# Optimization experiments

Hardware: AMD Instinct MI355X
Metric: run time of the kernel (lower is better)

## Reference

```python
import jax, jax.numpy as jnp
import numpy as np
import math

D_MODEL = 1024
N_HEADS = 16
HEAD_DIM = D_MODEL // N_HEADS


def setup_inputs() -> dict:
    key = jax.random.key(0)
    k1, k2, k3 = jax.random.split(key, 3)
    B, T = 2, 2048
    x = jax.random.normal(k1, (B, T, D_MODEL), dtype=jnp.float32)
    W_qkv = jax.random.normal(k2, (D_MODEL, 3 * D_MODEL), dtype=jnp.float32) * (1.0 / math.sqrt(D_MODEL))
    W_out = jax.random.normal(k3, (D_MODEL, D_MODEL), dtype=jnp.float32) * (1.0 / math.sqrt(D_MODEL))
    return {"x": x, "W_qkv": W_qkv, "W_out": W_out}


def reference(x, W_qkv, W_out):
    B, T, C = x.shape
    qkv = x @ W_qkv  # [B, T, 3C]
    q, k, v = jnp.split(qkv, 3, axis=-1)

    def heads(t):  # [B,T,C] -> [B,H,T,Dh]
        return t.reshape(B, T, N_HEADS, HEAD_DIM).transpose(0, 2, 1, 3)

    q, k, v = heads(q), heads(k), heads(v)
    scale = 1.0 / math.sqrt(HEAD_DIM)
    scores = jnp.einsum('bhtd,bhsd->bhts', q, k) * scale  # [B,H,T,T]
    causal = jnp.tril(jnp.ones((T, T), dtype=bool))
    scores = jnp.where(causal[None, None, :, :], scores, -jnp.inf)
    attn = jax.nn.softmax(scores, axis=-1)
    out = jnp.einsum('bhts,bhsd->bhtd', attn, v)  # [B,H,T,Dh]
    out = out.transpose(0, 2, 1, 3).reshape(B, T, C)
    return out @ W_out
```

## Files before the change

### kernel.cpp

```cpp
#include <hip/hip_runtime.h>
#include <hip/hip_bf16.h>

typedef __bf16 bf16;
typedef bf16 bf16x4 __attribute__((ext_vector_type(4)));
typedef bf16 bf16x8 __attribute__((ext_vector_type(8)));
typedef float f32x4 __attribute__((ext_vector_type(4)));

#define GLOAD16(g, l) __builtin_amdgcn_global_load_lds( \
    (const __attribute__((address_space(1))) void*)(g),  \
    (__attribute__((address_space(3))) void*)(l), 16, 0, 0)

#define EXP2F(x) __builtin_amdgcn_exp2f(x)
#define MFMA16(a, b, c) __builtin_amdgcn_mfma_f32_16x16x32_bf16(a, b, c, 0, 0, 0)

__global__ __launch_bounds__(256) void prep(const float* __restrict__ x,
                                            const float* __restrict__ Wqkv,
                                            const float* __restrict__ Wout,
                                            bf16* __restrict__ xb,
                                            bf16* __restrict__ wqkvT,
                                            bf16* __restrict__ woutT) {
  int id = blockIdx.x, tid = threadIdx.x;
  if (id < 2048) {
    int i = id * 256 + tid;
    const float4* p = (const float4*)x + (size_t)i * 2;
    float4 a = p[0], b = p[1];
    bf16x8 o;
    o[0] = (bf16)a.x; o[1] = (bf16)a.y; o[2] = (bf16)a.z; o[3] = (bf16)a.w;
    o[4] = (bf16)b.x; o[5] = (bf16)b.y; o[6] = (bf16)b.z; o[7] = (bf16)b.w;
    ((bf16x8*)xb)[i] = o;
  } else {
    __shared__ float tile[32][33];
    const float* src; bf16* dst; int N, j;
    if (id < 5120) { src = Wqkv; dst = wqkvT; N = 3072; j = id - 2048; }
    else           { src = Wout; dst = woutT; N = 1024; j = id - 5120; }
    int ntile = N / 32;
    int n0 = (j % ntile) * 32, k0 = (j / ntile) * 32;
    int tx = tid & 31, ty = tid >> 5;
#pragma unroll
    for (int i = 0; i < 4; i++)
      tile[ty + 8 * i][tx] = src[(size_t)(k0 + ty + 8 * i) * N + n0 + tx];
    __syncthreads();
#pragma unroll
    for (int i = 0; i < 4; i++)
      dst[(size_t)(n0 + ty + 8 * i) * 1024 + k0 + tx] = (bf16)tile[tx][ty + 8 * i];
  }
}

__device__ __forceinline__ void gemm_mainloop64(const bf16* __restrict__ A,
                                                const bf16* __restrict__ Bt,
                                                int K, int m0, int n0,
                                                f32x4 acc[4][4],
                                                bf16* As, bf16* Bs) {
  int tid = threadIdx.x;
  int lane = tid & 63;
  int wave = tid >> 6;
  int wr = wave >> 1, wc = wave & 1;
  int c16 = lane & 15, g = lane >> 4;
  f32x4 z = {0.f, 0.f, 0.f, 0.f};
#pragma unroll
  for (int m = 0; m < 4; m++)
#pragma unroll
    for (int n = 0; n < 4; n++) acc[m][n] = z;
  for (int k0 = 0; k0 < K; k0 += 64) {
#pragma unroll
    for (int i = 0; i < 4; i++) {
      int cc = tid + i * 256;
      int r = cc >> 3, ch = cc & 7;
      int sc = ch ^ (r & 7);
      GLOAD16(A + (size_t)(m0 + r) * K + k0 + sc * 8, As + cc * 8);
    }
#pragma unroll
    for (int i = 0; i < 4; i++) {
      int cc = tid + i * 256;
      int r = cc >> 3, ch = cc & 7;
      int sc = ch ^ (r & 7);
      GLOAD16(Bt + (size_t)(n0 + r) * K + k0 + sc * 8, Bs + cc * 8);
    }
    __syncthreads();
#pragma unroll
    for (int h = 0; h < 2; h++) {
      bf16x8 af[4], bfr[4];
#pragma unroll
      for (int m = 0; m < 4; m++) {
        int ar = wr * 64 + m * 16 + c16;
        af[m] = *(const bf16x8*)((const char*)As + ar * 128 + (((h * 4 + g) ^ (ar & 7)) << 4));
      }
#pragma unroll
      for (int n = 0; n < 4; n++) {
        int br = wc * 64 + n * 16 + c16;
        bfr[n] = *(const bf16x8*)((const char*)Bs + br * 128 + (((h * 4 + g) ^ (br & 7)) << 4));
      }
      __builtin_amdgcn_s_setprio(1);
#pragma unroll
      for (int m = 0; m < 4; m++)
#pragma unroll
        for (int n = 0; n < 4; n++)
          acc[m][n] = MFMA16(af[m], bfr[n], acc[m][n]);
      __builtin_amdgcn_s_setprio(0);
    }
    __syncthreads();
  }
}

__global__ __launch_bounds__(256) void gemm_qkv(const bf16* __restrict__ A,
                                                const bf16* __restrict__ Bt,
                                                bf16* __restrict__ q,
                                                bf16* __restrict__ kk,
                                                bf16* __restrict__ vt) {
  __shared__ bf16 As[128 * 64];
  __shared__ bf16 Bs[128 * 64];
  int id = blockIdx.x;
  int xc = id & 7, k = id >> 3;
  int bn = xc * 3 + (k % 3), bm = k / 3;
  int m0 = bm * 128, n0 = bn * 128;
  f32x4 acc[4][4];
  gemm_mainloop64(A, Bt, 1024, m0, n0, acc, As, Bs);
  int lane = threadIdx.x & 63;
  int wave = threadIdx.x >> 6;
  int wr = wave >> 1, wc = wave & 1;
  int c16 = lane & 15, g = lane >> 4;
  int which = n0 >> 10;
  const float QSCALE = 0.125f * 1.4426950408889634f;
  if (which == 2) {
#pragma unroll
    for (int m = 0; m < 4; m++)
#pragma unroll
      for (int n = 0; n < 4; n++) {
        int gm0 = m0 + wr * 64 + m * 16 + g * 4;
        int gn = n0 + wc * 64 + n * 16 + c16;
        int rem = gn & 1023, h = rem >> 6, d = rem & 63;
        int b = gm0 >> 11, t0 = gm0 & 2047;
        size_t bh = (size_t)(b * 16 + h);
        bf16x4 pv;
        pv[0] = (bf16)acc[m][n][0]; pv[1] = (bf16)acc[m][n][1];
        pv[2] = (bf16)acc[m][n][2]; pv[3] = (bf16)acc[m][n][3];
        *(bf16x4*)(vt + (bh * 64 + d) * 2048 + t0) = pv;
      }
  } else {
#pragma unroll
    for (int m = 0; m < 4; m++)
#pragma unroll
      for (int n = 0; n < 4; n++)
#pragma unroll
        for (int j = 0; j < 4; j++) {
          int gm = m0 + wr * 64 + m * 16 + g * 4 + j;
          int gn = n0 + wc * 64 + n * 16 + c16;
          int rem = gn & 1023, h = rem >> 6, d = rem & 63;
          int b = gm >> 11, t = gm & 2047;
          float v = acc[m][n][j];
          size_t bh = (size_t)(b * 16 + h);
          if (which == 0) q[(bh * 2048 + t) * 64 + d]  = (bf16)(v * QSCALE);
          else            kk[(bh * 2048 + t) * 64 + d] = (bf16)v;
        }
  }
}

__global__ __launch_bounds__(256) void gemm_out(const bf16* __restrict__ A,
                                                const bf16* __restrict__ Bt,
                                                float* __restrict__ C) {
  __shared__ bf16 As[64 * 64];
  __shared__ bf16 Bs[128 * 64];
  int tid = threadIdx.x;
  int lane = tid & 63;
  int wave = tid >> 6;
  int wr = wave >> 1, wc = wave & 1;
  int c16 = lane & 15, g = lane >> 4;
  int id = blockIdx.x;
  int bn = id & 7, bm = id >> 3;
  int m0 = bm * 64, n0 = bn * 128;
  const int K = 1024;
  f32x4 acc[2][4];
  {
    f32x4 z = {0.f, 0.f, 0.f, 0.f};
#pragma unroll
    for (int m = 0; m < 2; m++)
#pragma unroll
      for (int n = 0; n < 4; n++) acc[m][n] = z;
  }
  for (int k0 = 0; k0 < K; k0 += 64) {
#pragma unroll
    for (int i = 0; i < 2; i++) {
      int cc = tid + i * 256;
      int r = cc >> 3, ch = cc & 7;
      int sc = ch ^ (r & 7);
      GLOAD16(A + (size_t)(m0 + r) * K + k0 + sc * 8, As + cc * 8);
    }
#pragma unroll
    for (int i = 0; i < 4; i++) {
      int cc = tid + i * 256;
      int r = cc >> 3, ch = cc & 7;
      int sc = ch ^ (r & 7);
      GLOAD16(Bt + (size_t)(n0 + r) * K + k0 + sc * 8, Bs + cc * 8);
    }
    __syncthreads();
#pragma unroll
    for (int h = 0; h < 2; h++) {
      bf16x8 af[2], bfr[4];
#pragma unroll
      for (int m = 0; m < 2; m++) {
        int ar = wr * 32 + m * 16 + c16;
        af[m] = *(const bf16x8*)((const char*)As + ar * 128 + (((h * 4 + g) ^ (ar & 7)) << 4));
      }
#pragma unroll
      for (int n = 0; n < 4; n++) {
        int br = wc * 64 + n * 16 + c16;
        bfr[n] = *(const bf16x8*)((const char*)Bs + br * 128 + (((h * 4 + g) ^ (br & 7)) << 4));
      }
      __builtin_amdgcn_s_setprio(1);
#pragma unroll
      for (int m = 0; m < 2; m++)
#pragma unroll
        for (int n = 0; n < 4; n++)
          acc[m][n] = MFMA16(af[m], bfr[n], acc[m][n]);
      __builtin_amdgcn_s_setprio(0);
    }
    __syncthreads();
  }
#pragma unroll
  for (int m = 0; m < 2; m++)
#pragma unroll
    for (int n = 0; n < 4; n++)
#pragma unroll
      for (int j = 0; j < 4; j++) {
        int gm = m0 + wr * 32 + m * 16 + g * 4 + j;
        int gn = n0 + wc * 64 + n * 16 + c16;
        C[(size_t)gm * 1024 + gn] = acc[m][n][j];
      }
}

__global__ __launch_bounds__(512) void attn(const bf16* __restrict__ q,
                                            const bf16* __restrict__ kk,
                                            const bf16* __restrict__ vt,
                                            bf16* __restrict__ out) {
  __shared__ bf16 Ks[4][64 * 64];
  __shared__ bf16 Vs[4][64 * 64];
  __shared__ bf16 Ps[8 * 16 * 64];
  int tid = threadIdx.x, lane = tid & 63, w = tid >> 6;
  int c16 = lane & 15, g = (lane >> 4) & 3, g4 = g * 4;

  int id = blockIdx.x;
  int c = id & 7;
  int k = id >> 3;
  int s = k >> 5;
  int j5 = k & 31;
  int bxi = j5 & 15, b2 = j5 >> 4;
  int bx = s ? (15 - bxi) : bxi;
  int bh = 4 * c + 2 * b2 + s;
  int q0 = bx * 128;

  const bf16* qb = q  + (size_t)bh * 2048 * 64;
  const bf16* kb = kk + (size_t)bh * 2048 * 64;
  const bf16* vb = vt + (size_t)bh * 64 * 2048;
  int nt = 2 * bx + 2;
  int ns = nt >> 1;

  int qlo = q0 + w * 16;
  int qr = qlo + c16;
  bf16x8 qf[2];
#pragma unroll
  for (int ks = 0; ks < 2; ks++)
    qf[ks] = *(const bf16x8*)(qb + (size_t)(qlo + c16) * 64 + ks * 32 + g * 8);
  int r = tid >> 3;
  int swz = ((tid & 7) ^ (r & 7)) * 8;
  GLOAD16(kb + (size_t)r * 64 + swz, Ks[0] + tid * 8);
  GLOAD16(vb + (size_t)r * 2048 + swz, Vs[0] + tid * 8);
  GLOAD16(kb + (size_t)(64 + r) * 64 + swz, Ks[1] + tid * 8);
  GLOAD16(vb + (size_t)r * 2048 + 64 + swz, Vs[1] + tid * 8);
  __syncthreads();

  f32x4 o[4];
  float lrun = 0.f;
  {
    f32x4 z = {0.f, 0.f, 0.f, 0.f};
#pragma unroll
    for (int n = 0; n < 4; n++) o[n] = z;
  }
  bf16* Pw = Ps + w * 1024;

  auto QKT = [&](f32x4 S[4], const char* Kb) {
    {
      f32x4 z = {0.f, 0.f, 0.f, 0.f};
#pragma unroll
      for (int n = 0; n < 4; n++) S[n] = z;
    }
    __builtin_amdgcn_s_setprio(1);
#pragma unroll
    for (int ks = 0; ks < 2; ks++) {
      bf16x8 kf[4];
#pragma unroll
      for (int n = 0; n < 4; n++) {
        int srow = n * 16 + c16;
        kf[n] = *(const bf16x8*)(Kb + srow * 128 + (((ks * 4 + g) ^ (srow & 7)) << 4));
      }
#pragma unroll
      for (int n = 0; n < 4; n++)
        S[n] = MFMA16(kf[n], qf[ks], S[n]);
    }
    __builtin_amdgcn_s_setprio(0);
  };
  auto SMPV = [&](f32x4 S[4], int s0, const char* Vb) {
    if (s0 + 63 > qlo) {
#pragma unroll
      for (int n = 0; n < 4; n++)
#pragma unroll
        for (int rr = 0; rr < 4; rr++)
          if (s0 + n * 16 + g4 + rr > qr) S[n][rr] = -__builtin_inff();
    }
    float p[4][4];
    float rs = 0.f;
#pragma unroll
    for (int n = 0; n < 4; n++)
#pragma unroll
      for (int rr = 0; rr < 4; rr++) {
        p[n][rr] = EXP2F(S[n][rr]);
        rs += p[n][rr];
      }
    lrun += rs;
#pragma unroll
    for (int n = 0; n < 4; n++) {
      bf16x4 pw;
      pw[0] = (bf16)p[n][0]; pw[1] = (bf16)p[n][1];
      pw[2] = (bf16)p[n][2]; pw[3] = (bf16)p[n][3];
      *(bf16x4*)(Pw + c16 * 64 + (((2 * n + (g >> 1)) ^ (c16 & 7)) * 8) + (g & 1) * 4) = pw;
    }
    __builtin_amdgcn_s_setprio(1);
#pragma unroll
    for (int ks = 0; ks < 2; ks++) {
      bf16x8 vf[4];
#pragma unroll
      for (int n = 0; n < 4; n++) {
        int drow = n * 16 + c16;
        vf[n] = *(const bf16x8*)(Vb + drow * 128 + (((ks * 4 + g) ^ (drow & 7)) << 4));
      }
      bf16x8 pf = *(const bf16x8*)(Pw + c16 * 64 + (((ks * 4 + g) ^ (c16 & 7)) * 8));
#pragma unroll
      for (int n = 0; n < 4; n++)
        o[n] = MFMA16(pf, vf[n], o[n]);
    }
    __builtin_amdgcn_s_setprio(0);
  };

  for (int st = 0; st < ns; ++st) {
    if (st + 1 < ns) {
      int sn = st * 128 + 128;
      int nb = (2 * st + 2) & 3;
      GLOAD16(kb + (size_t)(sn + r) * 64 + swz, Ks[nb] + tid * 8);
      GLOAD16(vb + (size_t)r * 2048 + sn + swz, Vs[nb] + tid * 8);
      GLOAD16(kb + (size_t)(sn + 64 + r) * 64 + swz, Ks[nb + 1] + tid * 8);
      GLOAD16(vb + (size_t)r * 2048 + sn + 64 + swz, Vs[nb + 1] + tid * 8);
    }
    int t0 = 2 * st, t1 = 2 * st + 1;
    int s00 = t0 * 64, s01 = t1 * 64;
    bool c0 = (s00 <= qlo + 15), c1 = (s01 <= qlo + 15);
    f32x4 S0[4], S1[4];
    if (c0) QKT(S0, (const char*)Ks[t0 & 3]);
    if (c1) QKT(S1, (const char*)Ks[t1 & 3]);
    if (c0) SMPV(S0, s00, (const char*)Vs[t0 & 3]);
    if (c1) SMPV(S1, s01, (const char*)Vs[t1 & 3]);
    if (st + 1 < ns) {
      asm volatile("s_waitcnt vmcnt(0)" ::: "memory");
      __builtin_amdgcn_s_barrier();
      __builtin_amdgcn_sched_barrier(0);
    }
  }
  lrun += __shfl_xor(lrun, 16);
  lrun += __shfl_xor(lrun, 32);
  int b = bh >> 4, h = bh & 15;
#pragma unroll
  for (int j = 0; j < 4; j++) {
    float lv = __shfl(lrun, (lane & 48) | (g4 + j));
    float inv = 1.f / lv;
    int t = qlo + g4 + j;
#pragma unroll
    for (int n = 0; n < 4; n++) {
      int col = h * 64 + n * 16 + c16;
      out[((size_t)(b * 2048 + t)) * 1024 + col] = (bf16)(o[n][j] * inv);
    }
  }
}

extern "C" void kernel_launch(void* const* d_in, const int* in_sizes, int n_in,
                              void* d_out, int out_size, void* d_ws, size_t ws_size,
                              hipStream_t stream) {
  const float* x    = (const float*)d_in[0];
  const float* Wqkv = (const float*)d_in[1];
  const float* Wout = (const float*)d_in[2];
  float* outp = (float*)d_out;
  char* ws = (char*)d_ws;
  const size_t MB = 1024 * 1024;
  bf16* xb    = (bf16*)(ws);
  bf16* wqkvT = (bf16*)(ws + 8 * MB);
  bf16* woutT = (bf16*)(ws + 14 * MB);
  bf16* qb    = (bf16*)(ws + 16 * MB);
  bf16* kb    = (bf16*)(ws + 24 * MB);
  bf16* vtb   = (bf16*)(ws + 32 * MB);

  hipLaunchKernelGGL(prep, dim3(6144), dim3(256), 0, stream,
                     x, Wqkv, Wout, xb, wqkvT, woutT);
  hipLaunchKernelGGL(gemm_qkv, dim3(768), dim3(256), 0, stream,
                     xb, wqkvT, qb, kb, vtb);
  hipLaunchKernelGGL(attn, dim3(512), dim3(512), 0, stream,
                     qb, kb, vtb, xb);
  hipLaunchKernelGGL(gemm_out, dim3(512), dim3(256), 0, stream,
                     xb, woutT, outp);
}
```

Measured before the change: 95.77 us.

## Process 32 query rows per wave in attention with 4-wave blocks

The attention kernel now runs 4 waves per block instead of 8, and each wave handles two 16-row query tiles (32 rows). Every K and V fragment read from shared memory therefore feeds twice as many MFMAs, which halves the LDS read traffic per FLOP. Each thread now issues twice as many global-to-LDS loads. The cost is more accumulator registers per thread and fewer waves per block to hide latency, which may lower occupancy. The causal skip is also coarser, at 32-row granularity.

```diff
diff --git a/kernel.cpp b/kernel.cpp
--- a/kernel.cpp
+++ b/kernel.cpp
@@ -228,13 +228,13 @@
       }
 }
 
-__global__ __launch_bounds__(512) void attn(const bf16* __restrict__ q,
+__global__ __launch_bounds__(256) void attn(const bf16* __restrict__ q,
                                             const bf16* __restrict__ kk,
                                             const bf16* __restrict__ vt,
                                             bf16* __restrict__ out) {
   __shared__ bf16 Ks[4][64 * 64];
   __shared__ bf16 Vs[4][64 * 64];
-  __shared__ bf16 Ps[8 * 16 * 64];
+  __shared__ bf16 Ps[4 * 32 * 64];
   int tid = threadIdx.x, lane = tid & 63, w = tid >> 6;
   int c16 = lane & 15, g = (lane >> 4) & 3, g4 = g * 4;
 
@@ -254,127 +254,153 @@
   int nt = 2 * bx + 2;
   int ns = nt >> 1;
 
-  int qlo = q0 + w * 16;
-  int qr = qlo + c16;
-  bf16x8 qf[2];
-#pragma unroll
-  for (int ks = 0; ks < 2; ks++)
-    qf[ks] = *(const bf16x8*)(qb + (size_t)(qlo + c16) * 64 + ks * 32 + g * 8);
-  int r = tid >> 3;
-  int swz = ((tid & 7) ^ (r & 7)) * 8;
-  GLOAD16(kb + (size_t)r * 64 + swz, Ks[0] + tid * 8);
-  GLOAD16(vb + (size_t)r * 2048 + swz, Vs[0] + tid * 8);
-  GLOAD16(kb + (size_t)(64 + r) * 64 + swz, Ks[1] + tid * 8);
-  GLOAD16(vb + (size_t)r * 2048 + 64 + swz, Vs[1] + tid * 8);
+  int qlo = q0 + w * 32;
+  bf16x8 qf[2][2];
+#pragma unroll
+  for (int m = 0; m < 2; m++)
+#pragma unroll
+    for (int ks = 0; ks < 2; ks++)
+      qf[m][ks] = *(const bf16x8*)(qb + (size_t)(qlo + m * 16 + c16) * 64 + ks * 32 + g * 8);
+#pragma unroll
+  for (int i = 0; i < 2; i++) {
+    int cc = tid + i * 256;
+    int r = cc >> 3;
+    int sw = ((cc & 7) ^ (r & 7)) * 8;
+    GLOAD16(kb + (size_t)r * 64 + sw, Ks[0] + cc * 8);
+    GLOAD16(vb + (size_t)r * 2048 + sw, Vs[0] + cc * 8);
+    GLOAD16(kb + (size_t)(64 + r) * 64 + sw, Ks[1] + cc * 8);
+    GLOAD16(vb + (size_t)r * 2048 + 64 + sw, Vs[1] + cc * 8);
+  }
   __syncthreads();
 
-  f32x4 o[4];
-  float lrun = 0.f;
+  f32x4 o[2][4];
+  float lrun[2] = {0.f, 0.f};
   {
     f32x4 z = {0.f, 0.f, 0.f, 0.f};
 #pragma unroll
-    for (int n = 0; n < 4; n++) o[n] = z;
-  }
-  bf16* Pw = Ps + w * 1024;
-
-  auto QKT = [&](f32x4 S[4], const char* Kb) {
-    {
-      f32x4 z = {0.f, 0.f, 0.f, 0.f};
-#pragma unroll
-      for (int n = 0; n < 4; n++) S[n] = z;
-    }
-    __builtin_amdgcn_s_setprio(1);
-#pragma unroll
-    for (int ks = 0; ks < 2; ks++) {
-      bf16x8 kf[4];
-#pragma unroll
-      for (int n = 0; n < 4; n++) {
-        int srow = n * 16 + c16;
-        kf[n] = *(const bf16x8*)(Kb + srow * 128 + (((ks * 4 + g) ^ (srow & 7)) << 4));
-      }
-#pragma unroll
-      for (int n = 0; n < 4; n++)
-        S[n] = MFMA16(kf[n], qf[ks], S[n]);
-    }
-    __builtin_amdgcn_s_setprio(0);
-  };
-  auto SMPV = [&](f32x4 S[4], int s0, const char* Vb) {
-    if (s0 + 63 > qlo) {
-#pragma unroll
-      for (int n = 0; n < 4; n++)
-#pragma unroll
-        for (int rr = 0; rr < 4; rr++)
-          if (s0 + n * 16 + g4 + rr > qr) S[n][rr] = -__builtin_inff();
-    }
-    float p[4][4];
-    float rs = 0.f;
-#pragma unroll
-    for (int n = 0; n < 4; n++)
-#pragma unroll
-      for (int rr = 0; rr < 4; rr++) {
-        p[n][rr] = EXP2F(S[n][rr]);
-        rs += p[n][rr];
-      }
-    lrun += rs;
-#pragma unroll
-    for (int n = 0; n < 4; n++) {
-      bf16x4 pw;
-      pw[0] = (bf16)p[n][0]; pw[1] = (bf16)p[n][1];
-      pw[2] = (bf16)p[n][2]; pw[3] = (bf16)p[n][3];
-      *(bf16x4*)(Pw + c16 * 64 + (((2 * n + (g >> 1)) ^ (c16 & 7)) * 8) + (g & 1) * 4) = pw;
-    }
-    __builtin_amdgcn_s_setprio(1);
-#pragma unroll
-    for (int ks = 0; ks < 2; ks++) {
-      bf16x8 vf[4];
-#pragma unroll
-      for (int n = 0; n < 4; n++) {
-        int drow = n * 16 + c16;
-        vf[n] = *(const bf16x8*)(Vb + drow * 128 + (((ks * 4 + g) ^ (drow & 7)) << 4));
-      }
-      bf16x8 pf = *(const bf16x8*)(Pw + c16 * 64 + (((ks * 4 + g) ^ (c16 & 7)) * 8));
-#pragma unroll
-      for (int n = 0; n < 4; n++)
-        o[n] = MFMA16(pf, vf[n], o[n]);
-    }
-    __builtin_amdgcn_s_setprio(0);
-  };
+    for (int m = 0; m < 2; m++)
+#pragma unroll
+      for (int n = 0; n < 4; n++) o[m][n] = z;
+  }
+  bf16* Pw = Ps + w * 2048;
 
   for (int st = 0; st < ns; ++st) {
     if (st + 1 < ns) {
       int sn = st * 128 + 128;
       int nb = (2 * st + 2) & 3;
-      GLOAD16(kb + (size_t)(sn + r) * 64 + swz, Ks[nb] + tid * 8);
-      GLOAD16(vb + (size_t)r * 2048 + sn + swz, Vs[nb] + tid * 8);
-      GLOAD16(kb + (size_t)(sn + 64 + r) * 64 + swz, Ks[nb + 1] + tid * 8);
-      GLOAD16(vb + (size_t)r * 2048 + sn + 64 + swz, Vs[nb + 1] + tid * 8);
-    }
-    int t0 = 2 * st, t1 = 2 * st + 1;
-    int s00 = t0 * 64, s01 = t1 * 64;
-    bool c0 = (s00 <= qlo + 15), c1 = (s01 <= qlo + 15);
-    f32x4 S0[4], S1[4];
-    if (c0) QKT(S0, (const char*)Ks[t0 & 3]);
-    if (c1) QKT(S1, (const char*)Ks[t1 & 3]);
-    if (c0) SMPV(S0, s00, (const char*)Vs[t0 & 3]);
-    if (c1) SMPV(S1, s01, (const char*)Vs[t1 & 3]);
+#pragma unroll
+      for (int i = 0; i < 2; i++) {
+        int cc = tid + i * 256;
+        int r = cc >> 3;
+        int sw = ((cc & 7) ^ (r & 7)) * 8;
+        GLOAD16(kb + (size_t)(sn + r) * 64 + sw, Ks[nb] + cc * 8);
+        GLOAD16(vb + (size_t)r * 2048 + sn + sw, Vs[nb] + cc * 8);
+        GLOAD16(kb + (size_t)(sn + 64 + r) * 64 + sw, Ks[nb + 1] + cc * 8);
+        GLOAD16(vb + (size_t)r * 2048 + sn + 64 + sw, Vs[nb + 1] + cc * 8);
+      }
+    }
+#pragma unroll
+    for (int half = 0; half < 2; ++half) {
+      int t = 2 * st + half;
+      int s0 = t * 64;
+      if (s0 > qlo + 31) continue;
+      const char* Kb = (const char*)Ks[t & 3];
+      const char* Vb = (const char*)Vs[t & 3];
+      f32x4 S[2][4];
+      {
+        f32x4 z = {0.f, 0.f, 0.f, 0.f};
+#pragma unroll
+        for (int m = 0; m < 2; m++)
+#pragma unroll
+          for (int n = 0; n < 4; n++) S[m][n] = z;
+      }
+      __builtin_amdgcn_s_setprio(1);
+#pragma unroll
+      for (int ks = 0; ks < 2; ks++) {
+        bf16x8 kf[4];
+#pragma unroll
+        for (int n = 0; n < 4; n++) {
+          int srow = n * 16 + c16;
+          kf[n] = *(const bf16x8*)(Kb + srow * 128 + (((ks * 4 + g) ^ (srow & 7)) << 4));
+        }
+#pragma unroll
+        for (int m = 0; m < 2; m++)
+#pragma unroll
+          for (int n = 0; n < 4; n++)
+            S[m][n] = MFMA16(kf[n], qf[m][ks], S[m][n]);
+      }
+      __builtin_amdgcn_s_setprio(0);
+      bool diag = (s0 + 63 > qlo);
+#pragma unroll
+      for (int m = 0; m < 2; m++) {
+        int qr = qlo + m * 16 + c16;
+        if (diag) {
+#pragma unroll
+          for (int n = 0; n < 4; n++)
+#pragma unroll
+            for (int rr = 0; rr < 4; rr++)
+              if (s0 + n * 16 + g4 + rr > qr) S[m][n][rr] = -__builtin_inff();
+        }
+        float p[4][4];
+        float rs = 0.f;
+#pragma unroll
+        for (int n = 0; n < 4; n++)
+#pragma unroll
+          for (int rr = 0; rr < 4; rr++) {
+            p[n][rr] = EXP2F(S[m][n][rr]);
+            rs += p[n][rr];
+          }
+        lrun[m] += rs;
+        int rp = m * 16 + c16;
+#pragma unroll
+        for (int n = 0; n < 4; n++) {
+          bf16x4 pw;
+          pw[0] = (bf16)p[n][0]; pw[1] = (bf16)p[n][1];
+          pw[2] = (bf16)p[n][2]; pw[3] = (bf16)p[n][3];
+          *(bf16x4*)(Pw + rp * 64 + (((2 * n + (g >> 1)) ^ (c16 & 7)) * 8) + (g & 1) * 4) = pw;
+        }
+      }
+      __builtin_amdgcn_s_setprio(1);
+#pragma unroll
+      for (int ks = 0; ks < 2; ks++) {
+        bf16x8 vf[4];
+#pragma unroll
+        for (int n = 0; n < 4; n++) {
+          int drow = n * 16 + c16;
+          vf[n] = *(const bf16x8*)(Vb + drow * 128 + (((ks * 4 + g) ^ (drow & 7)) << 4));
+        }
+#pragma unroll
+        for (int m = 0; m < 2; m++) {
+          bf16x8 pf = *(const bf16x8*)(Pw + (m * 16 + c16) * 64 + (((ks * 4 + g) ^ (c16 & 7)) * 8));
+#pragma unroll
+          for (int n = 0; n < 4; n++)
+            o[m][n] = MFMA16(pf, vf[n], o[m][n]);
+        }
+      }
+      __builtin_amdgcn_s_setprio(0);
+    }
     if (st + 1 < ns) {
       asm volatile("s_waitcnt vmcnt(0)" ::: "memory");
       __builtin_amdgcn_s_barrier();
       __builtin_amdgcn_sched_barrier(0);
     }
   }
-  lrun += __shfl_xor(lrun, 16);
-  lrun += __shfl_xor(lrun, 32);
   int b = bh >> 4, h = bh & 15;
 #pragma unroll
-  for (int j = 0; j < 4; j++) {
-    float lv = __shfl(lrun, (lane & 48) | (g4 + j));
-    float inv = 1.f / lv;
-    int t = qlo + g4 + j;
-#pragma unroll
-    for (int n = 0; n < 4; n++) {
-      int col = h * 64 + n * 16 + c16;
-      out[((size_t)(b * 2048 + t)) * 1024 + col] = (bf16)(o[n][j] * inv);
+  for (int m = 0; m < 2; m++) {
+    float lm = lrun[m];
+    lm += __shfl_xor(lm, 16);
+    lm += __shfl_xor(lm, 32);
+#pragma unroll
+    for (int j = 0; j < 4; j++) {
+      float lv = __shfl(lm, (lane & 48) | (g4 + j));
+      float inv = 1.f / lv;
+      int t = qlo + m * 16 + g4 + j;
+#pragma unroll
+      for (int n = 0; n < 4; n++) {
+        int col = h * 64 + n * 16 + c16;
+        out[((size_t)(b * 2048 + t)) * 1024 + col] = (bf16)(o[m][n][j] * inv);
+      }
     }
   }
 }
@@ -399,7 +425,7 @@
                      x, Wqkv, Wout, xb, wqkvT, woutT);
   hipLaunchKernelGGL(gemm_qkv, dim3(768), dim3(256), 0, stream,
                      xb, wqkvT, qb, kb, vtb);
-  hipLaunchKernelGGL(attn, dim3(512), dim3(512), 0, stream,
+  hipLaunchKernelGGL(attn, dim3(512), dim3(256), 0, stream,
                      qb, kb, vtb, xb);
   hipLaunchKernelGGL(gemm_out, dim3(512), dim3(256), 0, stream,
                      xb, woutT, outp);
```

After: 103.2 us. 7.8% more time.
